# Optimization experiments

Hardware: AMD Instinct MI355X
Metric: run time of the kernel (lower is better)

Reference implementation:

```python
import jax, jax.numpy as jnp
import numpy as np

B, H, W, C = 32, 112, 112, 192
KH = KW = 3


def setup_inputs() -> dict:
    key = jax.random.key(0)
    k1, k2 = jax.random.split(key)
    x = jax.random.normal(k1, (B, H, W, C), dtype=jnp.float32)
    # depthwise kernel, HWIO with I=1 and feature_group_count=C (depth_multiplier=1)
    w = jax.random.normal(k2, (KH, KW, 1, C), dtype=jnp.float32) * 0.1
    b = jnp.zeros((C,), dtype=jnp.float32)
    return {"x": x, "w": w, "b": b}


def reference(x, w, b):
    # Depthwise conv = grouped conv with feature_group_count == channels_in.
    # stride 1, 'same' padding, dilation 1, depth_multiplier 1, linear activation.
    out = jax.lax.conv_general_dilated(
        x, w,
        window_strides=(1, 1),
        padding='SAME',
        rhs_dilation=(1, 1),
        dimension_numbers=('NHWC', 'HWIO', 'NHWC'),
        feature_group_count=C,
    )
    return out + b  # bias broadcast over channel axis
```

## Files before the change

kernel.cpp:

```cpp
#include <hip/hip_runtime.h>


constexpr int Bn = 32, Hn = 112, Wn = 112, Cn = 192, C4 = 48;
constexpr int WT = 16, CT = 16;
constexpr int WTiles = 7, CTiles = 3;
constexpr int NSTEP = 14, HG = 2;
constexpr int LWC = 18;
constexpr int ROWF4 = LWC * CT;
constexpr int REGF4 = 4 * ROWF4;
constexpr int REGB = REGF4 * 16;
constexpr int NSLOT = 3;

typedef float floatx4 __attribute__((ext_vector_type(4)));

__device__ __forceinline__ floatx4 fma4(floatx4 a, floatx4 b, floatx4 c) {
  c.x = fmaf(a.x, b.x, c.x);
  c.y = fmaf(a.y, b.y, c.y);
  c.z = fmaf(a.z, b.z, c.z);
  c.w = fmaf(a.w, b.w, c.w);
  return c;
}

__global__ __launch_bounds__(256, 2) void dwconv3x3_stream2(
    const float* __restrict__ x,
    const float* __restrict__ wgt,
    const float* __restrict__ bias,
    float* __restrict__ out) {
  __shared__ floatx4 lds[NSLOT * REGF4];
  const int tid = (int)threadIdx.x;
  const int lane = tid & 63;
  const int wave = tid >> 6;

  int bid = blockIdx.x;
  int chk = gridDim.x >> 3;
  int sbid = (bid & 7) * chk + (bid >> 3);
  int c4t = sbid % CTiles; int tt = sbid / CTiles;
  int wt = tt % WTiles;    tt /= WTiles;
  int hg = tt % HG;        int b = tt / HG;

  const int hbase = hg * (4 * NSTEP);
  const int w0 = wt * WT;
  const int cbase = c4t * (CT * 4);
  const float* xb = x + (long)b * Hn * Wn * Cn;
  const int rstr = Wn * Cn;

  const int cstart = (wave < 2) ? wave * 5 : 10 + (wave - 2) * 4;
  const int ccount = (wave < 2) ? 5 : 4;
  int rr[5];
  int colOff[5];
#pragma unroll
  for (int j = 0; j < 5; ++j) {
    int c = cstart + j;
    int l = c * 64 + lane;
    int r = l / ROWF4;
    int rem = l - r * ROWF4;
    int wi = rem >> 4, c4l = rem & 15;
    int wg = w0 + wi - 1;
    int wc = min(max(wg, 0), Wn - 1);
    rr[j] = r;
    colOff[j] = wc * Cn + cbase + c4l * 4;
  }

  for (int c = wave; c < 27; c += 4) {
    bool pre = c < 9;
    int cc = pre ? c : c - 9;
    int l = cc * 64 + lane;
    int r = l / ROWF4;
    int rem = l - r * ROWF4;
    int wi = rem >> 4, c4l = rem & 15;
    int row = pre ? r : 2 + r;
    int h = hbase + row - 1;
    int hc = min(max(h, 0), Hn - 1);
    int wg = w0 + wi - 1;
    int wc = min(max(wg, 0), Wn - 1);
    const float* src = xb + (long)hc * rstr + wc * Cn + cbase + c4l * 4;
    char* dst = (char*)lds +
        (pre ? (2 * REGB + 2 * ROWF4 * 16 + cc * 1024) : (cc * 1024));
    __builtin_amdgcn_global_load_lds(
        (const __attribute__((address_space(1))) void*)src,
        (__attribute__((address_space(3))) void*)dst, 16, 0, 0);
  }

  const int c4i = tid & 15;
  const int wi1 = tid >> 4;
  const int cofs = cbase + c4i * 4;
  const int wg1 = w0 + wi1;
  const float cs0 = (wg1 >= 1) ? 1.f : 0.f;
  const float cs2 = (wg1 <= Wn - 2) ? 1.f : 0.f;
  floatx4 wv[3][3];
#pragma unroll
  for (int kh = 0; kh < 3; ++kh) {
#pragma unroll
    for (int kw = 0; kw < 3; ++kw)
      wv[kh][kw] = *(const floatx4*)(wgt + (kh * 3 + kw) * Cn + cofs);
    wv[kh][0] *= cs0;
    wv[kh][2] *= cs2;
  }
  const floatx4 bv = *(const floatx4*)(bias + cofs);
  const float sTop = (hg == 0) ? 0.f : 1.f;
  const float sBot = (hg == HG - 1) ? 0.f : 1.f;

  const int ostr = Wn * C4;
  floatx4* outp = (floatx4*)out +
      ((long)b * Hn + hbase) * ostr + (long)wg1 * C4 + c4t * CT + c4i;
  const int ldaddr = wi1 * CT + c4i;

#pragma unroll
  for (int t = 0; t < NSTEP; ++t) {
    if (t < NSTEP - 1) {
      char* rbase = (char*)lds + ((t + 1) % 3) * REGB;
      const int R0 = 4 * (t + 1) + 2;
#pragma unroll
      for (int j = 0; j < 5; ++j) {
        if (j < ccount) {
          int h = hbase + R0 + rr[j] - 1;
          int hc = min(h, Hn - 1);
          const float* src = xb + (long)hc * rstr + colOff[j];
          __builtin_amdgcn_global_load_lds(
              (const __attribute__((address_space(1))) void*)src,
              (__attribute__((address_space(3))) void*)(rbase + (cstart + j) * 1024),
              16, 0, 0);
        }
      }
    }
    if (t == 0) {
      if (wave < 2) asm volatile("s_waitcnt vmcnt(5)" ::: "memory");
      else          asm volatile("s_waitcnt vmcnt(4)" ::: "memory");
    } else if (t < NSTEP - 1) {
      if (wave < 2) asm volatile("s_waitcnt vmcnt(9)" ::: "memory");
      else          asm volatile("s_waitcnt vmcnt(8)" ::: "memory");
    } else {
      asm volatile("s_waitcnt vmcnt(4)" ::: "memory");
    }
    __builtin_amdgcn_s_barrier();

    floatx4 acc[4];
#pragma unroll
    for (int o = 0; o < 4; ++o) acc[o] = bv;

#pragma unroll
    for (int r = 0; r < 6; ++r) {
      const int slot = (r < 2) ? (t + 2) % 3 : t % 3;
      const int rowoff = (r < 2) ? r + 2 : r - 2;
      const floatx4* base = lds + slot * REGF4 + rowoff * ROWF4 + ldaddr;
      floatx4 xv0 = base[0];
      floatx4 xv1 = base[CT];
      floatx4 xv2 = base[2 * CT];
      if (t == 0 && r == 0) { xv0 *= sTop; xv1 *= sTop; xv2 *= sTop; }
      if (t == NSTEP - 1 && r == 5) { xv0 *= sBot; xv1 *= sBot; xv2 *= sBot; }
#pragma unroll
      for (int kh = 0; kh < 3; ++kh) {
        int o = r - kh;
        if (o >= 0 && o < 4) {
          acc[o] = fma4(xv0, wv[kh][0], acc[o]);
          acc[o] = fma4(xv1, wv[kh][1], acc[o]);
          acc[o] = fma4(xv2, wv[kh][2], acc[o]);
        }
      }
    }

#pragma unroll
    for (int o = 0; o < 4; ++o)
      __builtin_nontemporal_store(acc[o], outp + (long)(4 * t + o) * ostr);

    __builtin_amdgcn_s_barrier();
  }
}

extern "C" void kernel_launch(void* const* d_in, const int* in_sizes, int n_in,
                              void* d_out, int out_size, void* d_ws, size_t ws_size,
                              hipStream_t stream) {
  const float* x = (const float*)d_in[0];
  const float* w = (const float*)d_in[1];
  const float* b = (const float*)d_in[2];
  float* out = (float*)d_out;

  const int grid = Bn * HG * WTiles * CTiles;
  dwconv3x3_stream2<<<grid, 256, 0, stream>>>(x, w, b, out);
}
```

Measured before the change: 114.7 us.

## Halve channel tile and block size, deepen LDS prefetch ring to four slots

Cuts the channel tile from 16 to 8 float4s and the block from 256 to 128 threads, doubling the grid. The LDS staging changes from a 3-slot rolling buffer with split halo handling to a 4-slot ring of full 4-row regions. Loads now run three steps ahead, with vmcnt waits retuned to match. The aim is more bytes in flight per block and more resident blocks to hide global latency. The cost is narrower per-row memory segments, some redundant halo-row loads, and more blocks.

```diff
diff --git a/kernel.cpp b/kernel.cpp
--- a/kernel.cpp
+++ b/kernel.cpp
@@ -2,16 +2,18 @@
 
 
 constexpr int Bn = 32, Hn = 112, Wn = 112, Cn = 192, C4 = 48;
-constexpr int WT = 16, CT = 16;
-constexpr int WTiles = 7, CTiles = 3;
+constexpr int WT = 16, CT = 8;
+constexpr int WTiles = 7, CTiles = 6;
 constexpr int NSTEP = 14, HG = 2;
 constexpr int LWC = 18;
 constexpr int ROWF4 = LWC * CT;
 constexpr int REGF4 = 4 * ROWF4;
 constexpr int REGB = REGF4 * 16;
-constexpr int NSLOT = 3;
+constexpr int NSLOT = 4;
 
 typedef float floatx4 __attribute__((ext_vector_type(4)));
+
+#define VMWAIT(n) asm volatile("s_waitcnt vmcnt(" #n ")" ::: "memory")
 
 __device__ __forceinline__ floatx4 fma4(floatx4 a, floatx4 b, floatx4 c) {
   c.x = fmaf(a.x, b.x, c.x);
@@ -21,7 +23,7 @@
   return c;
 }
 
-__global__ __launch_bounds__(256, 2) void dwconv3x3_stream2(
+__global__ __launch_bounds__(128, 2) void dwconv3x3_deep(
     const float* __restrict__ x,
     const float* __restrict__ wgt,
     const float* __restrict__ bias,
@@ -44,45 +46,39 @@
   const float* xb = x + (long)b * Hn * Wn * Cn;
   const int rstr = Wn * Cn;
 
-  const int cstart = (wave < 2) ? wave * 5 : 10 + (wave - 2) * 4;
-  const int ccount = (wave < 2) ? 5 : 4;
-  int rr[5];
-  int colOff[5];
+  const int cstart = wave * 5;
+  const int ccount = 5 - wave;
+  int rr[5], colOff[5];
 #pragma unroll
   for (int j = 0; j < 5; ++j) {
-    int c = cstart + j;
-    int l = c * 64 + lane;
+    int l = (cstart + j) * 64 + lane;
     int r = l / ROWF4;
     int rem = l - r * ROWF4;
-    int wi = rem >> 4, c4l = rem & 15;
+    int wi = rem >> 3, c4l = rem & 7;
     int wg = w0 + wi - 1;
     int wc = min(max(wg, 0), Wn - 1);
     rr[j] = r;
     colOff[j] = wc * Cn + cbase + c4l * 4;
   }
 
-  for (int c = wave; c < 27; c += 4) {
-    bool pre = c < 9;
-    int cc = pre ? c : c - 9;
-    int l = cc * 64 + lane;
-    int r = l / ROWF4;
-    int rem = l - r * ROWF4;
-    int wi = rem >> 4, c4l = rem & 15;
-    int row = pre ? r : 2 + r;
-    int h = hbase + row - 1;
-    int hc = min(max(h, 0), Hn - 1);
-    int wg = w0 + wi - 1;
-    int wc = min(max(wg, 0), Wn - 1);
-    const float* src = xb + (long)hc * rstr + wc * Cn + cbase + c4l * 4;
-    char* dst = (char*)lds +
-        (pre ? (2 * REGB + 2 * ROWF4 * 16 + cc * 1024) : (cc * 1024));
-    __builtin_amdgcn_global_load_lds(
-        (const __attribute__((address_space(1))) void*)src,
-        (__attribute__((address_space(3))) void*)dst, 16, 0, 0);
+#pragma unroll
+  for (int k = 0; k < 3; ++k) {
+#pragma unroll
+    for (int j = 0; j < 5; ++j) {
+      if (j < ccount) {
+        int h = hbase + 4 * k + rr[j] - 1;
+        int hc = min(max(h, 0), Hn - 1);
+        const float* src = xb + (long)hc * rstr + colOff[j];
+        char* dst = (char*)lds + k * REGB + (cstart + j) * 1024;
+        __builtin_amdgcn_global_load_lds(
+            (const __attribute__((address_space(1))) void*)src,
+            (__attribute__((address_space(3))) void*)dst, 16, 0, 0);
+      }
+    }
   }
 
-  const int c4i = tid & 15;
-  const int wi1 = tid >> 4;
+  const int c4i = tid & 7;
+  const int wi1 = tid >> 3;
   const int cofs = cbase + c4i * 4;
   const int wg1 = w0 + wi1;
   const float cs0 = (wg1 >= 1) ? 1.f : 0.f;
@@ -103,17 +99,16 @@
   const int ostr = Wn * C4;
   floatx4* outp = (floatx4*)out +
       ((long)b * Hn + hbase) * ostr + (long)wg1 * C4 + c4t * CT + c4i;
-  const int ldaddr = wi1 * CT + c4i;
 
 #pragma unroll
   for (int t = 0; t < NSTEP; ++t) {
-    if (t < NSTEP - 1) {
-      char* rbase = (char*)lds + ((t + 1) % 3) * REGB;
-      const int R0 = 4 * (t + 1) + 2;
+    if (t + 3 <= NSTEP) {
+      const int k = t + 3;
+      char* rbase = (char*)lds + (k & 3) * REGB;
 #pragma unroll
       for (int j = 0; j < 5; ++j) {
         if (j < ccount) {
-          int h = hbase + R0 + rr[j] - 1;
+          int h = hbase + 4 * k + rr[j] - 1;
           int hc = min(h, Hn - 1);
           const float* src = xb + (long)hc * rstr + colOff[j];
           __builtin_amdgcn_global_load_lds(
@@ -123,15 +118,11 @@
         }
       }
     }
-    if (t == 0) {
-      if (wave < 2) asm volatile("s_waitcnt vmcnt(5)" ::: "memory");
-      else          asm volatile("s_waitcnt vmcnt(4)" ::: "memory");
-    } else if (t < NSTEP - 1) {
-      if (wave < 2) asm volatile("s_waitcnt vmcnt(9)" ::: "memory");
-      else          asm volatile("s_waitcnt vmcnt(8)" ::: "memory");
-    } else {
-      asm volatile("s_waitcnt vmcnt(4)" ::: "memory");
-    }
+    if (t == 0)       { if (wave == 0) VMWAIT(10); else VMWAIT(8); }
+    else if (t == 1)  { if (wave == 0) VMWAIT(14); else VMWAIT(12); }
+    else if (t <= 11) { if (wave == 0) VMWAIT(18); else VMWAIT(16); }
+    else if (t == 12) { if (wave == 0) VMWAIT(13); else VMWAIT(12); }
+    else              { VMWAIT(8); }
     __builtin_amdgcn_s_barrier();
 
     floatx4 acc[4];
@@ -140,9 +131,9 @@
 
 #pragma unroll
     for (int r = 0; r < 6; ++r) {
-      const int slot = (r < 2) ? (t + 2) % 3 : t % 3;
-      const int rowoff = (r < 2) ? r + 2 : r - 2;
-      const floatx4* base = lds + slot * REGF4 + rowoff * ROWF4 + ldaddr;
+      const int reg = (r < 4) ? t : t + 1;
+      const int rowoff = (r < 4) ? r : r - 4;
+      const floatx4* base = lds + (reg & 3) * REGF4 + rowoff * ROWF4 + tid;
       floatx4 xv0 = base[0];
       floatx4 xv1 = base[CT];
       floatx4 xv2 = base[2 * CT];
@@ -176,5 +167,5 @@
   float* out = (float*)d_out;
 
   const int grid = Bn * HG * WTiles * CTiles;
-  dwconv3x3_stream2<<<grid, 256, 0, stream>>>(x, w, b, out);
+  dwconv3x3_deep<<<grid, 128, 0, stream>>>(x, w, b, out);
 }
```

After: 117.3 us. +2.3%, slower.

## Replace 3-slot region buffer with 8-row LDS ring and two-row steps

Applied to the files above, without the earlier changes.

The kernel now splits H into 4 groups of 28 rows and produces two output rows per step instead of four. Input rows go into an 8-slot ring of LDS rows with a prefetch depth of three steps, and the trailing barrier is removed because the ring depth guards against overwriting rows still being read. Launch bounds rise to 4 blocks per CU to raise occupancy, since per-block LDS shrinks. In exchange there is more halo re-reading across the extra H groups, and the vmcnt counts become more intricate, so any mistake in them would cause a data race.

```diff
diff --git a/kernel.cpp b/kernel.cpp
--- a/kernel.cpp
+++ b/kernel.cpp
@@ -4,14 +4,15 @@
 constexpr int Bn = 32, Hn = 112, Wn = 112, Cn = 192, C4 = 48;
 constexpr int WT = 16, CT = 16;
 constexpr int WTiles = 7, CTiles = 3;
-constexpr int NSTEP = 14, HG = 2;
+constexpr int NSTEP = 14, HG = 4;
 constexpr int LWC = 18;
 constexpr int ROWF4 = LWC * CT;
-constexpr int REGF4 = 4 * ROWF4;
-constexpr int REGB = REGF4 * 16;
-constexpr int NSLOT = 3;
+constexpr int ROWB = ROWF4 * 16;
+constexpr int NSLOT = 8;
 
 typedef float floatx4 __attribute__((ext_vector_type(4)));
+
+#define VMWAIT(n) asm volatile("s_waitcnt vmcnt(" #n ")" ::: "memory")
 
 __device__ __forceinline__ floatx4 fma4(floatx4 a, floatx4 b, floatx4 c) {
   c.x = fmaf(a.x, b.x, c.x);
@@ -21,12 +22,12 @@
   return c;
 }
 
-__global__ __launch_bounds__(256, 2) void dwconv3x3_stream2(
+__global__ __launch_bounds__(256, 4) void dwconv3x3_ring8(
     const float* __restrict__ x,
     const float* __restrict__ wgt,
     const float* __restrict__ bias,
     float* __restrict__ out) {
-  __shared__ floatx4 lds[NSLOT * REGF4];
+  __shared__ floatx4 lds[NSLOT * ROWF4];
   const int tid = (int)threadIdx.x;
   const int lane = tid & 63;
   const int wave = tid >> 6;
@@ -38,47 +39,60 @@
   int wt = tt % WTiles;    tt /= WTiles;
   int hg = tt % HG;        int b = tt / HG;
 
-  const int hbase = hg * (4 * NSTEP);
+  const int hbase = hg * (2 * NSTEP);
   const int w0 = wt * WT;
   const int cbase = c4t * (CT * 4);
   const float* xb = x + (long)b * Hn * Wn * Cn;
   const int rstr = Wn * Cn;
 
-  const int cstart = (wave < 2) ? wave * 5 : 10 + (wave - 2) * 4;
-  const int ccount = (wave < 2) ? 5 : 4;
-  int rr[5];
-  int colOff[5];
+  const int cstart2 = wave ? (1 + 2 * wave) : 0;
+  const int bcnt = wave ? 2 : 3;
+  int rr2[3], colOff2[3];
 #pragma unroll
-  for (int j = 0; j < 5; ++j) {
-    int c = cstart + j;
-    int l = c * 64 + lane;
-    int r = l / ROWF4;
-    int rem = l - r * ROWF4;
+  for (int j = 0; j < 3; ++j) {
+    int l = (cstart2 + j) * 64 + lane;
+    int r2 = (l >= ROWF4) ? 1 : 0;
+    int rem = l - r2 * ROWF4;
     int wi = rem >> 4, c4l = rem & 15;
     int wg = w0 + wi - 1;
     int wc = min(max(wg, 0), Wn - 1);
-    rr[j] = r;
-    colOff[j] = wc * Cn + cbase + c4l * 4;
+    rr2[j] = r2;
+    colOff2[j] = wc * Cn + cbase + c4l * 4;
   }
 
-  for (int c = wave; c < 27; c += 4) {
-    bool pre = c < 9;
-    int cc = pre ? c : c - 9;
-    int l = cc * 64 + lane;
-    int r = l / ROWF4;
-    int rem = l - r * ROWF4;
-    int wi = rem >> 4, c4l = rem & 15;
-    int row = pre ? r : 2 + r;
-    int h = hbase + row - 1;
-    int hc = min(max(h, 0), Hn - 1);
-    int wg = w0 + wi - 1;
-    int wc = min(max(wg, 0), Wn - 1);
-    const float* src = xb + (long)hc * rstr + wc * Cn + cbase + c4l * 4;
-    char* dst = (char*)lds +
-        (pre ? (2 * REGB + 2 * ROWF4 * 16 + cc * 1024) : (cc * 1024));
-    __builtin_amdgcn_global_load_lds(
-        (const __attribute__((address_space(1))) void*)src,
-        (__attribute__((address_space(3))) void*)dst, 16, 0, 0);
+  {
+    const int cstart4 = (wave < 2) ? wave * 5 : 10 + (wave - 2) * 4;
+    const int acnt = (wave < 2) ? 5 : 4;
+#pragma unroll
+    for (int j = 0; j < 5; ++j) {
+      if (j < acnt) {
+        int chunk = cstart4 + j;
+        int l = chunk * 64 + lane;
+        int r4 = l / ROWF4;
+        int rem = l - r4 * ROWF4;
+        int wi = rem >> 4, c4l = rem & 15;
+        int h = hbase + r4 - 1;
+        int hc = min(max(h, 0), Hn - 1);
+        int wg = w0 + wi - 1;
+        int wc = min(max(wg, 0), Wn - 1);
+        const float* src = xb + (long)hc * rstr + wc * Cn + cbase + c4l * 4;
+        char* dst = (char*)lds + chunk * 1024;
+        __builtin_amdgcn_global_load_lds(
+            (const __attribute__((address_space(1))) void*)src,
+            (__attribute__((address_space(3))) void*)dst, 16, 0, 0);
+      }
+    }
+#pragma unroll
+    for (int j = 0; j < 3; ++j) {
+      if (j < bcnt) {
+        int h = hbase + 4 + rr2[j] - 1;
+        const float* src = xb + (long)h * rstr + colOff2[j];
+        char* dst = (char*)lds + 4 * ROWB + (cstart2 + j) * 1024;
+        __builtin_amdgcn_global_load_lds(
+            (const __attribute__((address_space(1))) void*)src,
+            (__attribute__((address_space(3))) void*)dst, 16, 0, 0);
+      }
+    }
   }
 
   const int c4i = tid & 15;
@@ -103,55 +117,46 @@
   const int ostr = Wn * C4;
   floatx4* outp = (floatx4*)out +
       ((long)b * Hn + hbase) * ostr + (long)wg1 * C4 + c4t * CT + c4i;
-  const int ldaddr = wi1 * CT + c4i;
 
 #pragma unroll
   for (int t = 0; t < NSTEP; ++t) {
-    if (t < NSTEP - 1) {
-      char* rbase = (char*)lds + ((t + 1) % 3) * REGB;
-      const int R0 = 4 * (t + 1) + 2;
+    if (t == 0)       { if (wave == 0) VMWAIT(3); else VMWAIT(2); }
+    else if (t == 1)  { if (wave == 0) VMWAIT(5); else VMWAIT(4); }
+    else if (t < 13)  { if (wave == 0) VMWAIT(7); else VMWAIT(6); }
+    else              { VMWAIT(4); }
+    __builtin_amdgcn_s_barrier();
+
+    if (t <= 11) {
+      const int s0 = 2 * t + 6;
+      char* rbase = (char*)lds + (s0 & 7) * ROWB;
 #pragma unroll
-      for (int j = 0; j < 5; ++j) {
-        if (j < ccount) {
-          int h = hbase + R0 + rr[j] - 1;
+      for (int j = 0; j < 3; ++j) {
+        if (j < bcnt) {
+          int h = hbase + s0 + rr2[j] - 1;
           int hc = min(h, Hn - 1);
-          const float* src = xb + (long)hc * rstr + colOff[j];
+          const float* src = xb + (long)hc * rstr + colOff2[j];
           __builtin_amdgcn_global_load_lds(
               (const __attribute__((address_space(1))) void*)src,
-              (__attribute__((address_space(3))) void*)(rbase + (cstart + j) * 1024),
+              (__attribute__((address_space(3))) void*)(rbase + (cstart2 + j) * 1024),
               16, 0, 0);
         }
       }
     }
-    if (t == 0) {
-      if (wave < 2) asm volatile("s_waitcnt vmcnt(5)" ::: "memory");
-      else          asm volatile("s_waitcnt vmcnt(4)" ::: "memory");
-    } else if (t < NSTEP - 1) {
-      if (wave < 2) asm volatile("s_waitcnt vmcnt(9)" ::: "memory");
-      else          asm volatile("s_waitcnt vmcnt(8)" ::: "memory");
-    } else {
-      asm volatile("s_waitcnt vmcnt(4)" ::: "memory");
-    }
-    __builtin_amdgcn_s_barrier();
 
-    floatx4 acc[4];
+    floatx4 acc[2] = {bv, bv};
 #pragma unroll
-    for (int o = 0; o < 4; ++o) acc[o] = bv;
-
-#pragma unroll
-    for (int r = 0; r < 6; ++r) {
-      const int slot = (r < 2) ? (t + 2) % 3 : t % 3;
-      const int rowoff = (r < 2) ? r + 2 : r - 2;
-      const floatx4* base = lds + slot * REGF4 + rowoff * ROWF4 + ldaddr;
+    for (int r = 0; r < 4; ++r) {
+      const int slot = (2 * t + r) & 7;
+      const floatx4* base = lds + slot * ROWF4 + tid;
       floatx4 xv0 = base[0];
       floatx4 xv1 = base[CT];
       floatx4 xv2 = base[2 * CT];
       if (t == 0 && r == 0) { xv0 *= sTop; xv1 *= sTop; xv2 *= sTop; }
-      if (t == NSTEP - 1 && r == 5) { xv0 *= sBot; xv1 *= sBot; xv2 *= sBot; }
+      if (t == NSTEP - 1 && r == 3) { xv0 *= sBot; xv1 *= sBot; xv2 *= sBot; }
 #pragma unroll
-      for (int kh = 0; kh < 3; ++kh) {
-        int o = r - kh;
-        if (o >= 0 && o < 4) {
+      for (int o = 0; o < 2; ++o) {
+        int kh = r - o;
+        if (kh >= 0 && kh < 3) {
           acc[o] = fma4(xv0, wv[kh][0], acc[o]);
           acc[o] = fma4(xv1, wv[kh][1], acc[o]);
           acc[o] = fma4(xv2, wv[kh][2], acc[o]);
@@ -160,10 +165,8 @@
     }
 
 #pragma unroll
-    for (int o = 0; o < 4; ++o)
-      __builtin_nontemporal_store(acc[o], outp + (long)(4 * t + o) * ostr);
-
-    __builtin_amdgcn_s_barrier();
+    for (int o = 0; o < 2; ++o)
+      __builtin_nontemporal_store(acc[o], outp + (long)(2 * t + o) * ostr);
   }
 }
 
@@ -176,5 +179,5 @@
   float* out = (float*)d_out;
 
   const int grid = Bn * HG * WTiles * CTiles;
-  dwconv3x3_stream2<<<grid, 256, 0, stream>>>(x, w, b, out);
+  dwconv3x3_ring8<<<grid, 256, 0, stream>>>(x, w, b, out);
 }
```

Result: faster. 109.8 us (-4.2%).
